# Optimization experiments

Measured on AMD Instinct MI355X. Metric: run time of the kernel, lower is better.

## Reference

```python
import jax, jax.numpy as jnp
import numpy as np

N, E, IN, HID = 8192, 8192, 256, 256
DEG_P = 0.004  # avg degree ~32


def setup_inputs() -> dict:
    key = jax.random.key(0)
    ks = jax.random.split(key, 16)
    x = jax.random.normal(ks[0], (N, IN), dtype=jnp.float32)
    adj = (jax.random.uniform(ks[1], (N, N)) < DEG_P).astype(jnp.float32)
    tar_ei = jax.random.randint(ks[2], (2, E), 0, N, dtype=jnp.int32)
    s = 0.05
    return {
        'x': x, 'adj': adj, 'tar_ei': tar_ei,
        'W1c': jax.random.normal(ks[3], (IN, HID)) * s, 'b1c': jnp.zeros((HID,)),
        'W2c': jax.random.normal(ks[4], (HID, HID)) * s, 'b2c': jnp.zeros((HID,)),
        'W1j': jax.random.normal(ks[5], (IN, HID)) * s, 'b1j': jnp.zeros((HID,)),
        'W2j': jax.random.normal(ks[6], (HID, HID)) * s, 'b2j': jnp.zeros((HID,)),
        'Wl1': jax.random.normal(ks[7], (HID, HID)) * s, 'bl1': jnp.zeros((HID,)),
        'Wl2': jax.random.normal(ks[8], (HID, HID)) * s, 'bl2': jnp.zeros((HID,)),
        'Wout': jax.random.normal(ks[9], (HID, 1)) * s, 'bout': jnp.zeros((1,)),
    }


def _mlp2(h, W1, b1, W2, b2):
    # Linear -> ReLU -> (Dropout: eval-mode identity) -> Linear
    return jax.nn.relu(h @ W1 + b1) @ W2 + b2


def reference(x, adj, tar_ei, W1c, b1c, W2c, b2c, W1j, b1j, W2j, b2j,
              Wl1, bl1, Wl2, bl2, Wout, bout):
    beta = 1.0
    xi = x[tar_ei[0]]            # [E, IN]
    xj = x[tar_ei[1]]            # [E, IN]
    ai = adj[tar_ei[0]]          # [E, N] gathered adjacency rows
    aj = adj[tar_ei[1]]          # [E, N]
    # common-neighbor overlap + spmm_add aggregation: cn = ai*aj; xcn = cn @ x
    xcn = (ai * aj) @ x          # [E, IN]
    xij = _mlp2(xi * xj, W1j, b1j, W2j, b2j)
    xcn = _mlp2(xcn, W1c, b1c, W2c, b2c)
    h = beta * xcn + xij
    h = jax.nn.relu(h @ Wl1 + bl1)
    h = jax.nn.relu(h @ Wl2 + bl2)
    out = h @ Wout + bout        # [E, 1]
    return out.squeeze()
```

## Files before the change

kernel.cpp:

```cpp
#include <hip/hip_runtime.h>
#include <stdint.h>

#define NN 8192
#define NE 8192
#define DIM 256
#define NW 128
#define HCAP 64

typedef short bf16x8 __attribute__((ext_vector_type(8)));
typedef float f32x4 __attribute__((ext_vector_type(4)));

__device__ __forceinline__ unsigned short f2bf(float f) {
  uint32_t u = __builtin_bit_cast(uint32_t, f);
  u += 0x7fffu + ((u >> 16) & 1u);
  return (unsigned short)(u >> 16);
}
__device__ __forceinline__ float bf2f(unsigned short h) {
  uint32_t u = ((uint32_t)h) << 16;
  return __builtin_bit_cast(float, u);
}

__global__ __launch_bounds__(256) void prep_kernel(
    const float* __restrict__ adj,
    const float* __restrict__ W1c, const float* __restrict__ W2c,
    const float* __restrict__ W1j, const float* __restrict__ W2j,
    const float* __restrict__ Wl1, const float* __restrict__ Wl2,
    unsigned short* __restrict__ Wt,
    unsigned long long* __restrict__ bits) {
  const int blk = blockIdx.x;
  if (blk < 1536) {
    const float* Ws[6] = {W1c, W2c, W1j, W2j, Wl1, Wl2};
    const int w = blk >> 8;
    const int n = blk & 255;
    const int k = threadIdx.x;
    Wt[w * 65536 + n * DIM + k] = f2bf(Ws[w][k * DIM + n]);
  } else {
    const float4* __restrict__ adjv = (const float4*)adj;
    const int lane = threadIdx.x & 63;
    const int wv = (blk - 1536) * 4 + (threadIdx.x >> 6);
    const int nwv = 4096 * 4;
    const int total = NN * 32;
    for (int t = 2 * wv; t < total; t += 2 * nwv) {
      const int t1 = t + 1;
      float4 v0 = adjv[(size_t)(t >> 5) * 2048 + (t & 31) * 64 + lane];
      float4 v1 = adjv[(size_t)(t1 >> 5) * 2048 + (t1 & 31) * 64 + lane];
      unsigned long long m0 = __ballot(v0.x != 0.0f);
      unsigned long long m1 = __ballot(v0.y != 0.0f);
      unsigned long long m2 = __ballot(v0.z != 0.0f);
      unsigned long long m3 = __ballot(v0.w != 0.0f);
      unsigned long long n0 = __ballot(v1.x != 0.0f);
      unsigned long long n1 = __ballot(v1.y != 0.0f);
      unsigned long long n2 = __ballot(v1.z != 0.0f);
      unsigned long long n3 = __ballot(v1.w != 0.0f);
      if (lane == 0) {
        unsigned long long* p0 = bits + (size_t)(t >> 5) * NW + (t & 31) * 4;
        unsigned long long* p1 = bits + (size_t)(t1 >> 5) * NW + (t1 & 31) * 4;
        p0[0] = m0; p0[1] = m1; p0[2] = m2; p0[3] = m3;
        p1[0] = n0; p1[1] = n1; p1[2] = n2; p1[3] = n3;
      }
    }
  }
}


#define LDP 264

__device__ __forceinline__ void zero22(f32x4 a[2][2]) {
#pragma unroll
  for (int m = 0; m < 2; ++m)
#pragma unroll
    for (int n = 0; n < 2; ++n) {
      f32x4 z = {0.f, 0.f, 0.f, 0.f};
      a[m][n] = z;
    }
}

__device__ __forceinline__ void do_gemm(const unsigned short (*src)[LDP],
                                        const unsigned short* __restrict__ Wt,
                                        f32x4 acc[2][2], int lane, int wave) {
  const int lr = lane & 15;
  const int kl = (lane >> 4) * 8;
  const int n0 = wave * 32;
#pragma unroll
  for (int kk = 0; kk < 8; ++kk) {
    const int k0 = kk * 32 + kl;
    bf16x8 a0 = *(const bf16x8*)(&src[lr][k0]);
    bf16x8 a1 = *(const bf16x8*)(&src[16 + lr][k0]);
    bf16x8 b0 = *(const bf16x8*)(Wt + (size_t)(n0 + lr) * DIM + k0);
    bf16x8 b1 = *(const bf16x8*)(Wt + (size_t)(n0 + 16 + lr) * DIM + k0);
    acc[0][0] = __builtin_amdgcn_mfma_f32_16x16x32_bf16(a0, b0, acc[0][0], 0, 0, 0);
    acc[0][1] = __builtin_amdgcn_mfma_f32_16x16x32_bf16(a0, b1, acc[0][1], 0, 0, 0);
    acc[1][0] = __builtin_amdgcn_mfma_f32_16x16x32_bf16(a1, b0, acc[1][0], 0, 0, 0);
    acc[1][1] = __builtin_amdgcn_mfma_f32_16x16x32_bf16(a1, b1, acc[1][1], 0, 0, 0);
  }
}

__device__ __forceinline__ void epilogue(f32x4 acc[2][2],
                                         const float* __restrict__ bias,
                                         bool relu, unsigned short (*dst)[LDP],
                                         int lane, int wave) {
  const int lc = lane & 15;
  const int rg = (lane >> 4) * 4;
#pragma unroll
  for (int n = 0; n < 2; ++n) {
    const int col = wave * 32 + n * 16 + lc;
    const float bb = bias[col];
#pragma unroll
    for (int m = 0; m < 2; ++m)
#pragma unroll
      for (int q = 0; q < 4; ++q) {
        float v = acc[m][n][q] + bb;
        if (relu) v = fmaxf(v, 0.f);
        dst[m * 16 + rg + q][col] = f2bf(v);
      }
  }
}

__global__ __launch_bounds__(512) void fused_kernel(
    const float* __restrict__ x,
    const unsigned long long* __restrict__ bits,
    const int* __restrict__ tar,
    const unsigned short* __restrict__ Wt,
    const float* __restrict__ b1c, const float* __restrict__ b2c,
    const float* __restrict__ b1j, const float* __restrict__ b2j,
    const float* __restrict__ bl1, const float* __restrict__ bl2,
    const float* __restrict__ Wout, const float* __restrict__ bout,
    float* __restrict__ out) {
  __shared__ unsigned short lA[32][LDP];
  __shared__ unsigned short lB[32][LDP];
  __shared__ unsigned short lC[32][LDP];
  __shared__ int hits[32][HCAP];
  __shared__ int nh[32];
  __shared__ int ii[32], jj[32];

  const int tid = threadIdx.x;
  const int lane = tid & 63;
  const int wave = tid >> 6;
  const int e0 = blockIdx.x * 32;

  if (tid < 32) {
    ii[tid] = tar[e0 + tid];
    jj[tid] = tar[NE + e0 + tid];
    nh[tid] = 0;
  }
  __syncthreads();

  {
    const int e = tid >> 4;
    const int t16 = tid & 15;
    const unsigned long long* bi = bits + (size_t)ii[e] * NW + t16 * 8;
    const unsigned long long* bj = bits + (size_t)jj[e] * NW + t16 * 8;
#pragma unroll
    for (int q = 0; q < 8; ++q) {
      unsigned long long m = bi[q] & bj[q];
      const int w = t16 * 8 + q;
      const int base = (w >> 2) << 8;
      const int qq = w & 3;
      while (m) {
        int b = __builtin_ctzll(m);
        m &= m - 1;
        int idx = atomicAdd(&nh[e], 1);
        if (idx < HCAP) hits[e][idx] = base + (b << 2) + qq;
      }
    }
  }
  __syncthreads();

  {
    const int col = tid & 255;
    const int sub = tid >> 8;
#pragma unroll
    for (int p = 0; p < 16; ++p) {
      const int e = p * 2 + sub;
      const int n = nh[e] < HCAP ? nh[e] : HCAP;
      float xc = 0.f;
      for (int h = 0; h < n; ++h)
        xc += x[(size_t)hits[e][h] * DIM + col];
      const float vi = x[(size_t)ii[e] * DIM + col];
      const float vj = x[(size_t)jj[e] * DIM + col];
      lA[e][col] = f2bf(xc);
      lC[e][col] = f2bf(vi * vj);
    }
  }
  __syncthreads();

  f32x4 acc[2][2], pAcc[2][2];

  zero22(acc);
  do_gemm(lA, Wt + 0 * 65536, acc, lane, wave);
  epilogue(acc, b1c, true, lB, lane, wave);
  __syncthreads();

  zero22(pAcc);
  do_gemm(lB, Wt + 1 * 65536, pAcc, lane, wave);
  zero22(acc);
  do_gemm(lC, Wt + 2 * 65536, acc, lane, wave);
  epilogue(acc, b1j, true, lA, lane, wave);
  __syncthreads();

  do_gemm(lA, Wt + 3 * 65536, pAcc, lane, wave);
  {
    const int lc = lane & 15;
    const int rg = (lane >> 4) * 4;
#pragma unroll
    for (int n = 0; n < 2; ++n) {
      const int col = wave * 32 + n * 16 + lc;
      const float bb = b2c[col] + b2j[col];
#pragma unroll
      for (int m = 0; m < 2; ++m)
#pragma unroll
        for (int q = 0; q < 4; ++q)
          lB[m * 16 + rg + q][col] = f2bf(pAcc[m][n][q] + bb);
    }
  }
  __syncthreads();

  zero22(acc);
  do_gemm(lB, Wt + 4 * 65536, acc, lane, wave);
  epilogue(acc, bl1, true, lA, lane, wave);
  __syncthreads();

  zero22(acc);
  do_gemm(lA, Wt + 5 * 65536, acc, lane, wave);
  epilogue(acc, bl2, true, lB, lane, wave);
  __syncthreads();

  const int el = tid >> 4;
  const int part = tid & 15;
  float s = 0.f;
#pragma unroll
  for (int q = 0; q < 16; ++q) {
    const int c = part * 16 + q;
    s += bf2f(lB[el][c]) * Wout[c];
  }
#pragma unroll
  for (int o = 8; o; o >>= 1) s += __shfl_xor(s, o);
  if (part == 0) out[e0 + el] = s + bout[0];
}

extern "C" void kernel_launch(void* const* d_in, const int* in_sizes, int n_in,
                              void* d_out, int out_size, void* d_ws, size_t ws_size,
                              hipStream_t stream) {
  const float* x    = (const float*)d_in[0];
  const float* adj  = (const float*)d_in[1];
  const int*   tar  = (const int*)d_in[2];
  const float* W1c  = (const float*)d_in[3];
  const float* b1c  = (const float*)d_in[4];
  const float* W2c  = (const float*)d_in[5];
  const float* b2c  = (const float*)d_in[6];
  const float* W1j  = (const float*)d_in[7];
  const float* b1j  = (const float*)d_in[8];
  const float* W2j  = (const float*)d_in[9];
  const float* b2j  = (const float*)d_in[10];
  const float* Wl1  = (const float*)d_in[11];
  const float* bl1  = (const float*)d_in[12];
  const float* Wl2  = (const float*)d_in[13];
  const float* bl2  = (const float*)d_in[14];
  const float* Wout = (const float*)d_in[15];
  const float* bout = (const float*)d_in[16];

  char* ws = (char*)d_ws;
  unsigned short*     Wt   = (unsigned short*)(ws);
  unsigned long long* bits = (unsigned long long*)(ws + (1u << 20));

  prep_kernel<<<1536 + 4096, 256, 0, stream>>>(adj, W1c, W2c, W1j, W2j, Wl1,
                                               Wl2, Wt, bits);

  fused_kernel<<<NE / 32, 512, 0, stream>>>(x, bits, tar, Wt, b1c, b2c, b1j,
                                            b2j, bl1, bl2, Wout, bout,
                                            (float*)d_out);
}
```

Measured before the change: 88.12 us.

## Prefetch GEMM weights into registers one stage ahead and hoist loads

```diff
diff --git a/kernel.cpp b/kernel.cpp
--- a/kernel.cpp
+++ b/kernel.cpp
@@ -6,6 +6,7 @@
 #define DIM 256
 #define NW 128
 #define HCAP 64
+#define TE 32
 
 typedef short bf16x8 __attribute__((ext_vector_type(8)));
 typedef float f32x4 __attribute__((ext_vector_type(4)));
@@ -65,46 +66,55 @@
 
 #define LDP 264
 
-__device__ __forceinline__ void zero22(f32x4 a[2][2]) {
-#pragma unroll
-  for (int m = 0; m < 2; ++m)
-#pragma unroll
-    for (int n = 0; n < 2; ++n) {
-      f32x4 z = {0.f, 0.f, 0.f, 0.f};
-      a[m][n] = z;
-    }
-}
-
-__device__ __forceinline__ void do_gemm(const unsigned short (*src)[LDP],
-                                        const unsigned short* __restrict__ Wt,
-                                        f32x4 acc[2][2], int lane, int wave) {
+__device__ __forceinline__ void load_w(const unsigned short* __restrict__ Wt,
+                                       bf16x8 w[2][8], int lane, int wave) {
   const int lr = lane & 15;
   const int kl = (lane >> 4) * 8;
   const int n0 = wave * 32;
+#pragma unroll
+  for (int kk = 0; kk < 8; ++kk) {
+    const int k0 = kk * 32 + kl;
+    w[0][kk] = *(const bf16x8*)(Wt + (size_t)(n0 + lr) * DIM + k0);
+    w[1][kk] = *(const bf16x8*)(Wt + (size_t)(n0 + 16 + lr) * DIM + k0);
+  }
+}
+
+__device__ __forceinline__ void gemm_reg(const unsigned short (*src)[LDP],
+                                         const bf16x8 w[2][8],
+                                         f32x4 acc[2][2], int lane) {
+  const int lr = lane & 15;
+  const int kl = (lane >> 4) * 8;
 #pragma unroll
   for (int kk = 0; kk < 8; ++kk) {
     const int k0 = kk * 32 + kl;
     bf16x8 a0 = *(const bf16x8*)(&src[lr][k0]);
     bf16x8 a1 = *(const bf16x8*)(&src[16 + lr][k0]);
-    bf16x8 b0 = *(const bf16x8*)(Wt + (size_t)(n0 + lr) * DIM + k0);
-    bf16x8 b1 = *(const bf16x8*)(Wt + (size_t)(n0 + 16 + lr) * DIM + k0);
-    acc[0][0] = __builtin_amdgcn_mfma_f32_16x16x32_bf16(a0, b0, acc[0][0], 0, 0, 0);
-    acc[0][1] = __builtin_amdgcn_mfma_f32_16x16x32_bf16(a0, b1, acc[0][1], 0, 0, 0);
-    acc[1][0] = __builtin_amdgcn_mfma_f32_16x16x32_bf16(a1, b0, acc[1][0], 0, 0, 0);
-    acc[1][1] = __builtin_amdgcn_mfma_f32_16x16x32_bf16(a1, b1, acc[1][1], 0, 0, 0);
-  }
-}
-
-__device__ __forceinline__ void epilogue(f32x4 acc[2][2],
-                                         const float* __restrict__ bias,
-                                         bool relu, unsigned short (*dst)[LDP],
-                                         int lane, int wave) {
+    acc[0][0] = __builtin_amdgcn_mfma_f32_16x16x32_bf16(a0, w[0][kk], acc[0][0], 0, 0, 0);
+    acc[0][1] = __builtin_amdgcn_mfma_f32_16x16x32_bf16(a0, w[1][kk], acc[0][1], 0, 0, 0);
+    acc[1][0] = __builtin_amdgcn_mfma_f32_16x16x32_bf16(a1, w[0][kk], acc[1][0], 0, 0, 0);
+    acc[1][1] = __builtin_amdgcn_mfma_f32_16x16x32_bf16(a1, w[1][kk], acc[1][1], 0, 0, 0);
+  }
+}
+
+__device__ __forceinline__ void zero22(f32x4 a[2][2]) {
+#pragma unroll
+  for (int m = 0; m < 2; ++m)
+#pragma unroll
+    for (int n = 0; n < 2; ++n) {
+      f32x4 z = {0.f, 0.f, 0.f, 0.f};
+      a[m][n] = z;
+    }
+}
+
+__device__ __forceinline__ void epilogue32(f32x4 acc[2][2], float bb0, float bb1,
+                                           bool relu, unsigned short (*dst)[LDP],
+                                           int lane, int wave) {
   const int lc = lane & 15;
   const int rg = (lane >> 4) * 4;
 #pragma unroll
   for (int n = 0; n < 2; ++n) {
     const int col = wave * 32 + n * 16 + lc;
-    const float bb = bias[col];
+    const float bb = n ? bb1 : bb0;
 #pragma unroll
     for (int m = 0; m < 2; ++m)
 #pragma unroll
@@ -116,7 +126,7 @@
   }
 }
 
-__global__ __launch_bounds__(512) void fused_kernel(
+__global__ __launch_bounds__(512, 2) void fused_kernel(
     const float* __restrict__ x,
     const unsigned long long* __restrict__ bits,
     const int* __restrict__ tar,
@@ -126,60 +136,90 @@
     const float* __restrict__ bl1, const float* __restrict__ bl2,
     const float* __restrict__ Wout, const float* __restrict__ bout,
     float* __restrict__ out) {
-  __shared__ unsigned short lA[32][LDP];
-  __shared__ unsigned short lB[32][LDP];
-  __shared__ unsigned short lC[32][LDP];
-  __shared__ int hits[32][HCAP];
-  __shared__ int nh[32];
-  __shared__ int ii[32], jj[32];
+  __shared__ unsigned short lA[TE][LDP];
+  __shared__ unsigned short lB[TE][LDP];
+  __shared__ unsigned short lC[TE][LDP];
+  __shared__ int hits[TE][HCAP];
+  __shared__ int nh[TE];
 
   const int tid = threadIdx.x;
   const int lane = tid & 63;
   const int wave = tid >> 6;
-  const int e0 = blockIdx.x * 32;
-
-  if (tid < 32) {
-    ii[tid] = tar[e0 + tid];
-    jj[tid] = tar[NE + e0 + tid];
-    nh[tid] = 0;
-  }
-  __syncthreads();
-
+  const int e0 = blockIdx.x * TE;
+
+  const int lc = lane & 15;
+  const int c0 = wave * 32 + lc;
+  const int c1 = c0 + 16;
+  const float vb1c0 = b1c[c0], vb1c1 = b1c[c1];
+  const float vb1j0 = b1j[c0], vb1j1 = b1j[c1];
+  const float vb20 = b2c[c0] + b2j[c0], vb21 = b2c[c1] + b2j[c1];
+  const float vbl10 = bl1[c0], vbl11 = bl1[c1];
+  const float vbl20 = bl2[c0], vbl21 = bl2[c1];
+  const int gpart = tid & 15;
+  float wv[16];
+#pragma unroll
+  for (int q = 0; q < 16; ++q) wv[q] = Wout[gpart * 16 + q];
+  const float vbout = bout[0];
+
+  if (tid < TE) nh[tid] = 0;
+
+  const int e_a = tid >> 4;
+  const int t16 = tid & 15;
+  const int ia = tar[e0 + e_a];
+  const int ja = tar[NE + e0 + e_a];
+  unsigned long long bw_i[8], bw_j[8];
   {
-    const int e = tid >> 4;
-    const int t16 = tid & 15;
-    const unsigned long long* bi = bits + (size_t)ii[e] * NW + t16 * 8;
-    const unsigned long long* bj = bits + (size_t)jj[e] * NW + t16 * 8;
-#pragma unroll
-    for (int q = 0; q < 8; ++q) {
-      unsigned long long m = bi[q] & bj[q];
-      const int w = t16 * 8 + q;
-      const int base = (w >> 2) << 8;
-      const int qq = w & 3;
-      while (m) {
-        int b = __builtin_ctzll(m);
-        m &= m - 1;
-        int idx = atomicAdd(&nh[e], 1);
-        if (idx < HCAP) hits[e][idx] = base + (b << 2) + qq;
-      }
-    }
-  }
-  __syncthreads();
+    const unsigned long long* bi = bits + (size_t)ia * NW + t16 * 8;
+    const unsigned long long* bj = bits + (size_t)ja * NW + t16 * 8;
+#pragma unroll
+    for (int q = 0; q < 8; ++q) { bw_i[q] = bi[q]; bw_j[q] = bj[q]; }
+  }
 
   {
     const int col = tid & 255;
     const int sub = tid >> 8;
+    float vi[16], vj[16];
 #pragma unroll
     for (int p = 0; p < 16; ++p) {
-      const int e = p * 2 + sub;
+      const int e = sub * 16 + p;
+      vi[p] = x[(size_t)tar[e0 + e] * DIM + col];
+      vj[p] = x[(size_t)tar[NE + e0 + e] * DIM + col];
+    }
+#pragma unroll
+    for (int p = 0; p < 16; ++p)
+      lC[sub * 16 + p][col] = f2bf(vi[p] * vj[p]);
+  }
+  __syncthreads();
+
+#pragma unroll
+  for (int q = 0; q < 8; ++q) {
+    unsigned long long m = bw_i[q] & bw_j[q];
+    const int w = t16 * 8 + q;
+    const int base = (w >> 2) << 8;
+    const int qq = w & 3;
+    while (m) {
+      int b = __builtin_ctzll(m);
+      m &= m - 1;
+      int idx = atomicAdd(&nh[e_a], 1);
+      if (idx < HCAP) hits[e_a][idx] = base + (b << 2) + qq;
+    }
+  }
+  __syncthreads();
+
+  bf16x8 wX[2][8], wY[2][8];
+  load_w(Wt + 0 * 65536, wX, lane, wave);
+  load_w(Wt + 1 * 65536, wY, lane, wave);
+  {
+    const int col = tid & 255;
+    const int sub = tid >> 8;
+#pragma unroll
+    for (int p = 0; p < 16; ++p) {
+      const int e = sub * 16 + p;
       const int n = nh[e] < HCAP ? nh[e] : HCAP;
       float xc = 0.f;
       for (int h = 0; h < n; ++h)
         xc += x[(size_t)hits[e][h] * DIM + col];
-      const float vi = x[(size_t)ii[e] * DIM + col];
-      const float vj = x[(size_t)jj[e] * DIM + col];
       lA[e][col] = f2bf(xc);
-      lC[e][col] = f2bf(vi * vj);
     }
   }
   __syncthreads();
@@ -187,25 +227,27 @@
   f32x4 acc[2][2], pAcc[2][2];
 
   zero22(acc);
-  do_gemm(lA, Wt + 0 * 65536, acc, lane, wave);
-  epilogue(acc, b1c, true, lB, lane, wave);
+  gemm_reg(lA, wX, acc, lane);
+  load_w(Wt + 2 * 65536, wX, lane, wave);
+  epilogue32(acc, vb1c0, vb1c1, true, lB, lane, wave);
   __syncthreads();
 
   zero22(pAcc);
-  do_gemm(lB, Wt + 1 * 65536, pAcc, lane, wave);
+  gemm_reg(lB, wY, pAcc, lane);
+  load_w(Wt + 3 * 65536, wY, lane, wave);
   zero22(acc);
-  do_gemm(lC, Wt + 2 * 65536, acc, lane, wave);
-  epilogue(acc, b1j, true, lA, lane, wave);
-  __syncthreads();
-
-  do_gemm(lA, Wt + 3 * 65536, pAcc, lane, wave);
+  gemm_reg(lC, wX, acc, lane);
+  epilogue32(acc, vb1j0, vb1j1, true, lA, lane, wave);
+  __syncthreads();
+
+  gemm_reg(lA, wY, pAcc, lane);
+  load_w(Wt + 4 * 65536, wX, lane, wave);
   {
-    const int lc = lane & 15;
     const int rg = (lane >> 4) * 4;
 #pragma unroll
     for (int n = 0; n < 2; ++n) {
       const int col = wave * 32 + n * 16 + lc;
-      const float bb = b2c[col] + b2j[col];
+      const float bb = n ? vb21 : vb20;
 #pragma unroll
       for (int m = 0; m < 2; ++m)
 #pragma unroll
@@ -216,26 +258,24 @@
   __syncthreads();
 
   zero22(acc);
-  do_gemm(lB, Wt + 4 * 65536, acc, lane, wave);
-  epilogue(acc, bl1, true, lA, lane, wave);
+  gemm_reg(lB, wX, acc, lane);
+  load_w(Wt + 5 * 65536, wY, lane, wave);
+  epilogue32(acc, vbl10, vbl11, true, lA, lane, wave);
   __syncthreads();
 
   zero22(acc);
-  do_gemm(lA, Wt + 5 * 65536, acc, lane, wave);
-  epilogue(acc, bl2, true, lB, lane, wave);
+  gemm_reg(lA, wY, acc, lane);
+  epilogue32(acc, vbl20, vbl21, true, lB, lane, wave);
   __syncthreads();
 
   const int el = tid >> 4;
-  const int part = tid & 15;
   float s = 0.f;
 #pragma unroll
-  for (int q = 0; q < 16; ++q) {
-    const int c = part * 16 + q;
-    s += bf2f(lB[el][c]) * Wout[c];
-  }
+  for (int q = 0; q < 16; ++q)
+    s += bf2f(lB[el][gpart * 16 + q]) * wv[q];
 #pragma unroll
   for (int o = 8; o; o >>= 1) s += __shfl_xor(s, o);
-  if (part == 0) out[e0 + el] = s + bout[0];
+  if (gpart == 0) out[e0 + el] = s + vbout;
 }
 
 extern "C" void kernel_launch(void* const* d_in, const int* in_sizes, int n_in,
@@ -266,7 +306,7 @@
   prep_kernel<<<1536 + 4096, 256, 0, stream>>>(adj, W1c, W2c, W1j, W2j, Wl1,
                                                Wl2, Wt, bits);
 
-  fused_kernel<<<NE / 32, 512, 0, stream>>>(x, bits, tar, Wt, b1c, b2c, b1j,
+  fused_kernel<<<NE / TE, 512, 0, stream>>>(x, bits, tar, Wt, b1c, b2c, b1j,
                                             b2j, bl1, bl2, Wout, bout,
                                             (float*)d_out);
 }
```

After: 81.22 us. -7.8%, faster.
